# Performance work log

Hardware: AMD Instinct MI355X
Metric: run time of the kernel (lower is better)

The kernel has to match this reference:

```python
import jax, jax.numpy as jnp
import numpy as np

N = 50000      # nodes
E = 800000     # edges (before self-loops)
F_IN = 128
F_OUT = 128
H = 4          # heads
SLOPE = 0.2    # LeakyReLU negative slope (PyG GATConv default)


def setup_inputs() -> dict:
    key = jax.random.key(0)
    ks = jax.random.split(key, 8)
    x = jax.random.normal(ks[0], (N, F_IN), dtype=jnp.float32)
    edge_index = jax.random.randint(ks[1], (2, E), 0, N, dtype=jnp.int64)
    W = jax.random.normal(ks[2], (H, F_IN, F_OUT), dtype=jnp.float32) * (1.0 / np.sqrt(F_IN))
    att_src = jax.random.normal(ks[3], (H, F_OUT), dtype=jnp.float32) * (1.0 / np.sqrt(F_OUT))
    att_dst = jax.random.normal(ks[4], (H, F_OUT), dtype=jnp.float32) * (1.0 / np.sqrt(F_OUT))
    bias = jnp.zeros((H, F_OUT), dtype=jnp.float32)
    W_out = jax.random.normal(ks[5], (H * F_OUT, F_OUT), dtype=jnp.float32) * (1.0 / np.sqrt(H * F_OUT))
    b_out = jnp.zeros((F_OUT,), dtype=jnp.float32)
    return {"x": x, "edge_index": edge_index, "W": W, "att_src": att_src,
            "att_dst": att_dst, "bias": bias, "W_out": W_out, "b_out": b_out}


def _gat_head(x, src, dst, W_h, a_src, a_dst, b_h):
    # x: [N, F_in]; src/dst: [E'] edge endpoints (messages flow src -> dst)
    xW = x @ W_h                                   # [N, F_out]
    alpha_s = xW @ a_src                           # [N]
    alpha_d = xW @ a_dst                           # [N]
    logits = alpha_s[src] + alpha_d[dst]           # [E']
    logits = jnp.where(logits > 0, logits, SLOPE * logits)  # leaky_relu
    # segment softmax over edges grouped by destination node
    seg_max = jax.ops.segment_max(logits, dst, num_segments=N)  # [N]
    e = jnp.exp(logits - seg_max[dst])             # [E']
    denom = jax.ops.segment_sum(e, dst, num_segments=N)         # [N]
    alpha = e / denom[dst]                         # [E']
    # weighted scatter-aggregate of source features to destinations
    out = jax.ops.segment_sum(alpha[:, None] * xW[src], dst, num_segments=N)  # [N, F_out]
    return out + b_h


def reference(x, edge_index, W, att_src, att_dst, bias, W_out, b_out):
    # add self-loops (PyG GATConv default)
    loops = jnp.arange(N, dtype=edge_index.dtype)
    src = jnp.concatenate([edge_index[0], loops])
    dst = jnp.concatenate([edge_index[1], loops])
    heads = [_gat_head(x, src, dst, W[h], att_src[h], att_dst[h], bias[h]) for h in range(H)]
    h_cat = jnp.concatenate(heads, axis=1)         # [N, H*F_out]
    return jax.nn.relu(h_cat @ W_out + b_out)      # [N, F_out]
```

## Files before the change

### kernel.cpp

```cpp
#include <hip/hip_runtime.h>
#include <hip/hip_bf16.h>

constexpr int NN = 50000;
constexpr int EE = 800000;
constexpr float SLOPE = 0.2f;
constexpr int CAP = 48;
constexpr int ZE = NN * CAP;
constexpr int LDP = 520;

typedef __bf16 bf16x8 __attribute__((ext_vector_type(8)));
typedef __bf16 bf16x4 __attribute__((ext_vector_type(4)));
typedef float f32x4 __attribute__((ext_vector_type(4)));
typedef float f32x2 __attribute__((ext_vector_type(2)));

__device__ __forceinline__ int edge_at(const int* e32, const long long* e64, int use64, long i) {
    return use64 ? (int)e64[i] : e32[i];
}

__device__ __forceinline__ f32x2 bfpair(unsigned u) {
    f32x2 r;
    r.x = __uint_as_float(u << 16);
    r.y = __uint_as_float(u & 0xffff0000u);
    return r;
}

__global__ void k_prec(const float* __restrict__ W, const float* __restrict__ Wout,
                       const float* __restrict__ att_s, const float* __restrict__ att_d,
                       const float* __restrict__ bias, const float* __restrict__ bout,
                       const long long* e64, int* flag, int* cnt,
                       __bf16* __restrict__ Bfrag, float* __restrict__ wsv, float* __restrict__ wdv,
                       float* __restrict__ cvec, uint4* __restrict__ ew) {
    int b = blockIdx.x, t = threadIdx.x;
    if (b < 512) {
        int h = b >> 7, k = b & 127;
        float acc = 0.f;
        for (int j = 0; j < 128; j++) {
            float w = W[((size_t)(h * 128 + k)) * 128 + j];
            acc += w * Wout[((size_t)(h * 128 + j)) * 128 + t];
        }
        int K = h * 128 + k;
        int k0i = K >> 5, kb = (K >> 3) & 3, jj = K & 7;
        int ni = t >> 4, lr = t & 15;
        Bfrag[(((size_t)k0i * 8 + ni) * 64 + kb * 16 + lr) * 8 + jj] = (__bf16)acc;
    } else if (b == 512) {
        float acc = bout[t];
        for (int j = 0; j < 512; j++) acc += bias[j] * Wout[(size_t)j * 128 + t];
        cvec[t] = acc;
        if (t == 0) ew[ZE] = make_uint4(0u, 0u, 0u, 0u);
    } else if (b < 517) {
        int h = b - 513;
        float as = 0.f, ad = 0.f;
        for (int j = 0; j < 128; j++) {
            float w = W[((size_t)(h * 128 + t)) * 128 + j];
            as += w * att_s[h * 128 + j];
            ad += w * att_d[h * 128 + j];
        }
        wsv[h * 128 + t] = as;
        wdv[h * 128 + t] = ad;
    } else {
        int i = (b - 517) * 128 + t;
        if (i < NN) cnt[i] = 0;
        if (b == 517 && t < 64) {
            long long v = e64[t];
            bool ok = (v >= 0) && (v < (long long)NN);
            unsigned long long m = __ballot(ok);
            if (t == 0) *flag = (m == 0xFFFFFFFFFFFFFFFFull) ? 1 : 0;
        }
    }
}

__global__ __launch_bounds__(256) void k_prep(const float* __restrict__ x, const float* __restrict__ wsv,
                                              const float* __restrict__ wdv, __bf16* __restrict__ xb,
                                              float* __restrict__ as_, float* __restrict__ ad_) {
    int n = blockIdx.x * blockDim.x + threadIdx.x;
    if (n >= NN) return;
    const float4* xr = (const float4*)(x + (size_t)n * 128);
    __bf16* xo = xb + (size_t)n * 128;
    float s[4] = {0, 0, 0, 0}, d[4] = {0, 0, 0, 0};
    for (int q = 0; q < 32; q += 2) {
        float4 v0 = xr[q], v1 = xr[q + 1];
        bf16x8 o;
        o[0] = (__bf16)v0.x; o[1] = (__bf16)v0.y; o[2] = (__bf16)v0.z; o[3] = (__bf16)v0.w;
        o[4] = (__bf16)v1.x; o[5] = (__bf16)v1.y; o[6] = (__bf16)v1.z; o[7] = (__bf16)v1.w;
        *(bf16x8*)(xo + q * 4) = o;
        #pragma unroll
        for (int h = 0; h < 4; h++) {
            float4 a0 = ((const float4*)(wsv + h * 128))[q];
            float4 a1 = ((const float4*)(wsv + h * 128))[q + 1];
            float4 b0 = ((const float4*)(wdv + h * 128))[q];
            float4 b1 = ((const float4*)(wdv + h * 128))[q + 1];
            s[h] += v0.x * a0.x + v0.y * a0.y + v0.z * a0.z + v0.w * a0.w
                  + v1.x * a1.x + v1.y * a1.y + v1.z * a1.z + v1.w * a1.w;
            d[h] += v0.x * b0.x + v0.y * b0.y + v0.z * b0.z + v0.w * b0.w
                  + v1.x * b1.x + v1.y * b1.y + v1.z * b1.z + v1.w * b1.w;
        }
    }
    #pragma unroll
    for (int h = 0; h < 4; h++) { as_[n * 4 + h] = s[h]; ad_[n * 4 + h] = d[h]; }
}

__global__ __launch_bounds__(256) void k_scatterB(const int* e32, const long long* e64, const int* flag,
                                                  const float* __restrict__ as_, const float* __restrict__ ad_,
                                                  int* cnt, uint4* __restrict__ ew) {
    long i = (long)blockIdx.x * blockDim.x + threadIdx.x;
    if (i >= (long)EE + NN) return;
    int use64 = *flag;
    int s, d;
    if (i < EE) { s = edge_at(e32, e64, use64, i); d = edge_at(e32, e64, use64, (long)EE + i); }
    else        { s = (int)(i - EE); d = s; }
    float4 av = *(const float4*)(as_ + (size_t)s * 4);
    float4 bv = *(const float4*)(ad_ + (size_t)d * 4);
    float l0 = av.x + bv.x; l0 = l0 > 0.f ? l0 : SLOPE * l0;
    float l1 = av.y + bv.y; l1 = l1 > 0.f ? l1 : SLOPE * l1;
    float l2 = av.z + bv.z; l2 = l2 > 0.f ? l2 : SLOPE * l2;
    float l3 = av.w + bv.w; l3 = l3 > 0.f ? l3 : SLOPE * l3;
    bf16x4 w;
    w[0] = (__bf16)__expf(l0);
    w[1] = (__bf16)__expf(l1);
    w[2] = (__bf16)__expf(l2);
    w[3] = (__bf16)__expf(l3);
    uint2 wp = *(uint2*)&w;
    int pos = d * CAP + atomicAdd(&cnt[d], 1);
    ew[pos] = make_uint4((unsigned)s, wp.x, wp.y, 0u);
}

__global__ __launch_bounds__(256) void k_aggF(const int* __restrict__ cnt, const uint4* __restrict__ ew,
                                              const __bf16* __restrict__ xb, const __bf16* __restrict__ Bfrag,
                                              const float* __restrict__ cvec, float* __restrict__ y) {
    __shared__ __bf16 aggL[16 * LDP];
    int t = threadIdx.x;
    int lane = t & 63;
    int half = lane >> 5;
    int sub = lane & 31;
    int hw = ((t >> 6) << 1) + half;
    size_t fo = 4 * (size_t)sub;

    #pragma unroll
    for (int r = 0; r < 2; r++) {
        int nl = r * 8 + hw;
        int n = blockIdx.x * 16 + nl;
        int deg = cnt[n];
        int beg = n * CAP;
        int last = beg + deg - 1;
        int dmax = max(deg, __shfl_xor(deg, 32));
        int nit = (dmax + 3) >> 2;
        f32x2 a01[4] = {}, a23[4] = {};
        f32x2 dn01 = {0.f, 0.f}, dn23 = {0.f, 0.f};
        int e = beg;
        int i0 = (e     <= last) ? e     : ZE;
        int i1 = (e + 1 <= last) ? e + 1 : ZE;
        int i2 = (e + 2 <= last) ? e + 2 : ZE;
        int i3 = (e + 3 <= last) ? e + 3 : ZE;
        uint4 r0 = ew[i0], r1 = ew[i1], r2 = ew[i2], r3 = ew[i3];
        for (int it = 0; it < nit; ++it) {
            e += 4;
            int p0 = (e     <= last) ? e     : ZE;
            int p1 = (e + 1 <= last) ? e + 1 : ZE;
            int p2 = (e + 2 <= last) ? e + 2 : ZE;
            int p3 = (e + 3 <= last) ? e + 3 : ZE;
            uint4 n0 = ew[p0], n1 = ew[p1], n2 = ew[p2], n3 = ew[p3];
            uint2 x0 = *(const uint2*)(xb + (size_t)r0.x * 128 + fo);
            uint2 x1 = *(const uint2*)(xb + (size_t)r1.x * 128 + fo);
            uint2 x2 = *(const uint2*)(xb + (size_t)r2.x * 128 + fo);
            uint2 x3 = *(const uint2*)(xb + (size_t)r3.x * 128 + fo);
#define ACCP(R, XR) { \
            f32x2 w01 = bfpair(R.y), w23 = bfpair(R.z); \
            f32x2 x01 = bfpair(XR.x), x23 = bfpair(XR.y); \
            f32x2 q0 = {w01.x, w01.x}, q1 = {w01.y, w01.y}; \
            f32x2 q2 = {w23.x, w23.x}, q3 = {w23.y, w23.y}; \
            a01[0] += q0 * x01; a23[0] += q0 * x23; \
            a01[1] += q1 * x01; a23[1] += q1 * x23; \
            a01[2] += q2 * x01; a23[2] += q2 * x23; \
            a01[3] += q3 * x01; a23[3] += q3 * x23; \
            dn01 += w01; dn23 += w23; }
            ACCP(r0, x0) ACCP(r1, x1) ACCP(r2, x2) ACCP(r3, x3)
#undef ACCP
            r0 = n0; r1 = n1; r2 = n2; r3 = n3;
        }
        float inv[4];
        inv[0] = 1.f / dn01.x; inv[1] = 1.f / dn01.y;
        inv[2] = 1.f / dn23.x; inv[3] = 1.f / dn23.y;
        __bf16* ar = aggL + nl * LDP + fo;
        #pragma unroll
        for (int h = 0; h < 4; h++) {
            bf16x4 o;
            o[0] = (__bf16)(a01[h].x * inv[h]); o[1] = (__bf16)(a01[h].y * inv[h]);
            o[2] = (__bf16)(a23[h].x * inv[h]); o[3] = (__bf16)(a23[h].y * inv[h]);
            *(bf16x4*)(ar + h * 128) = o;
        }
    }
    __syncthreads();

    int w = t >> 6;
    int lr = lane & 15, kb = lane >> 4;
    f32x4 acc[2] = {};
    for (int k0i = 0; k0i < 16; k0i++) {
        bf16x8 a = *(const bf16x8*)(aggL + lr * LDP + k0i * 32 + kb * 8);
        #pragma unroll
        for (int ni = 0; ni < 2; ni++) {
            int ni_g = w * 2 + ni;
            bf16x8 b = *(const bf16x8*)(Bfrag + (((size_t)k0i * 8 + ni_g) * 64 + lane) * 8);
            acc[ni] = __builtin_amdgcn_mfma_f32_16x16x32_bf16(a, b, acc[ni], 0, 0, 0);
        }
    }
    int row0 = blockIdx.x * 16 + kb * 4;
    #pragma unroll
    for (int ni = 0; ni < 2; ni++) {
        int c = (w * 2 + ni) * 16 + lr;
        float cv = cvec[c];
        #pragma unroll
        for (int r = 0; r < 4; r++) {
            y[(size_t)(row0 + r) * 128 + c] = fmaxf(acc[ni][r] + cv, 0.f);
        }
    }
}

extern "C" void kernel_launch(void* const* d_in, const int* in_sizes, int n_in,
                              void* d_out, int out_size, void* d_ws, size_t ws_size,
                              hipStream_t stream) {
    const float* x     = (const float*)d_in[0];
    const void*  ei    = d_in[1];
    const float* W     = (const float*)d_in[2];
    const float* att_s = (const float*)d_in[3];
    const float* att_d = (const float*)d_in[4];
    const float* bias  = (const float*)d_in[5];
    const float* Wout  = (const float*)d_in[6];
    const float* bout  = (const float*)d_in[7];
    float* y = (float*)d_out;

    const int* e32 = (const int*)ei;
    const long long* e64 = (const long long*)ei;

    char* ws = (char*)d_ws;
    size_t off = 0;
    auto alloc = [&](size_t bytes) -> void* {
        void* p = ws + off;
        off = (off + bytes + 255) & ~(size_t)255;
        return p;
    };
    __bf16* xb    = (__bf16*)alloc((size_t)NN * 128 * 2);
    uint4* ew     = (uint4*)alloc(((size_t)NN * CAP + 1) * 16);
    float* as_    = (float*)alloc((size_t)NN * 4 * 4);
    float* ad_    = (float*)alloc((size_t)NN * 4 * 4);
    __bf16* Bfrag = (__bf16*)alloc((size_t)512 * 128 * 2);
    float* wsv    = (float*)alloc(4 * 128 * 4);
    float* wdv    = (float*)alloc(4 * 128 * 4);
    float* cvec   = (float*)alloc(128 * 4);
    int* cnt      = (int*)alloc((size_t)NN * 4);
    int* flag     = (int*)alloc(4);

    int precBlocks = 517 + (NN + 127) / 128;
    k_prec<<<precBlocks, 128, 0, stream>>>(W, Wout, att_s, att_d, bias, bout,
                                           e64, flag, cnt, Bfrag, wsv, wdv, cvec, ew);
    k_prep<<<(NN + 255) / 256, 256, 0, stream>>>(x, wsv, wdv, xb, as_, ad_);
    k_scatterB<<<(EE + NN + 255) / 256, 256, 0, stream>>>(e32, e64, flag, as_, ad_, cnt, ew);
    k_aggF<<<NN / 16, 256, 0, stream>>>(cnt, ew, xb, Bfrag, cvec, y);
}
```

Before: 139.3 us.

## Split edge scatter into index-only scatter plus per-node weight computation kernel

The edge scatter kernel now writes only the 4-byte source index into a per-destination slot array (capacity raised to 64, power-of-two indexing). A new kernel, one wavefront per destination node, reads those indices, gathers bf16 source attention scores, computes the exp-LeakyReLU weights, and writes the 16-byte edge records contiguously. This aims to make the random-atomic scatter pass lighter and turn weight writes into coalesced stores. In exchange it adds a kernel launch and an extra pass over the slots, stores source scores in bf16 (less precise), and uses more workspace for the larger capacity.

```diff
diff --git a/kernel.cpp b/kernel.cpp
--- a/kernel.cpp
+++ b/kernel.cpp
@@ -4,7 +4,7 @@
 constexpr int NN = 50000;
 constexpr int EE = 800000;
 constexpr float SLOPE = 0.2f;
-constexpr int CAP = 48;
+constexpr int CAP = 64;
 constexpr int ZE = NN * CAP;
 constexpr int LDP = 520;
 
@@ -71,7 +71,7 @@
 
 __global__ __launch_bounds__(256) void k_prep(const float* __restrict__ x, const float* __restrict__ wsv,
                                               const float* __restrict__ wdv, __bf16* __restrict__ xb,
-                                              float* __restrict__ as_, float* __restrict__ ad_) {
+                                              bf16x4* __restrict__ as_b, float* __restrict__ ad_) {
     int n = blockIdx.x * blockDim.x + threadIdx.x;
     if (n >= NN) return;
     const float4* xr = (const float4*)(x + (size_t)n * 128);
@@ -95,33 +95,47 @@
                   + v1.x * b1.x + v1.y * b1.y + v1.z * b1.z + v1.w * b1.w;
         }
     }
+    bf16x4 ab;
+    ab[0] = (__bf16)s[0]; ab[1] = (__bf16)s[1]; ab[2] = (__bf16)s[2]; ab[3] = (__bf16)s[3];
+    as_b[n] = ab;
     #pragma unroll
-    for (int h = 0; h < 4; h++) { as_[n * 4 + h] = s[h]; ad_[n * 4 + h] = d[h]; }
+    for (int h = 0; h < 4; h++) ad_[n * 4 + h] = d[h];
 }
 
 __global__ __launch_bounds__(256) void k_scatterB(const int* e32, const long long* e64, const int* flag,
-                                                  const float* __restrict__ as_, const float* __restrict__ ad_,
-                                                  int* cnt, uint4* __restrict__ ew) {
+                                                  int* cnt, int* __restrict__ colv) {
     long i = (long)blockIdx.x * blockDim.x + threadIdx.x;
     if (i >= (long)EE + NN) return;
     int use64 = *flag;
     int s, d;
     if (i < EE) { s = edge_at(e32, e64, use64, i); d = edge_at(e32, e64, use64, (long)EE + i); }
     else        { s = (int)(i - EE); d = s; }
-    float4 av = *(const float4*)(as_ + (size_t)s * 4);
-    float4 bv = *(const float4*)(ad_ + (size_t)d * 4);
-    float l0 = av.x + bv.x; l0 = l0 > 0.f ? l0 : SLOPE * l0;
-    float l1 = av.y + bv.y; l1 = l1 > 0.f ? l1 : SLOPE * l1;
-    float l2 = av.z + bv.z; l2 = l2 > 0.f ? l2 : SLOPE * l2;
-    float l3 = av.w + bv.w; l3 = l3 > 0.f ? l3 : SLOPE * l3;
+    int pos = (d << 6) + atomicAdd(&cnt[d], 1);
+    colv[pos] = s;
+}
+
+__global__ __launch_bounds__(256) void k_wcomp(const int* __restrict__ cnt, const int* __restrict__ colv,
+                                               const bf16x4* __restrict__ as_b, const float* __restrict__ ad_,
+                                               uint4* __restrict__ ew) {
+    int lane = threadIdx.x & 63;
+    int n = blockIdx.x * 4 + (threadIdx.x >> 6);
+    int deg = cnt[n];
+    if (lane >= deg) return;
+    int slot = (n << 6) + lane;
+    int src = colv[slot];
+    bf16x4 ab = as_b[src];
+    float4 adv = *(const float4*)(ad_ + (size_t)n * 4);
+    float l0 = (float)ab[0] + adv.x; l0 = l0 > 0.f ? l0 : SLOPE * l0;
+    float l1 = (float)ab[1] + adv.y; l1 = l1 > 0.f ? l1 : SLOPE * l1;
+    float l2 = (float)ab[2] + adv.z; l2 = l2 > 0.f ? l2 : SLOPE * l2;
+    float l3 = (float)ab[3] + adv.w; l3 = l3 > 0.f ? l3 : SLOPE * l3;
     bf16x4 w;
     w[0] = (__bf16)__expf(l0);
     w[1] = (__bf16)__expf(l1);
     w[2] = (__bf16)__expf(l2);
     w[3] = (__bf16)__expf(l3);
     uint2 wp = *(uint2*)&w;
-    int pos = d * CAP + atomicAdd(&cnt[d], 1);
-    ew[pos] = make_uint4((unsigned)s, wp.x, wp.y, 0u);
+    ew[slot] = make_uint4((unsigned)src, wp.x, wp.y, 0u);
 }
 
 __global__ __launch_bounds__(256) void k_aggF(const int* __restrict__ cnt, const uint4* __restrict__ ew,
@@ -140,7 +154,7 @@
         int nl = r * 8 + hw;
         int n = blockIdx.x * 16 + nl;
         int deg = cnt[n];
-        int beg = n * CAP;
+        int beg = n << 6;
         int last = beg + deg - 1;
         int dmax = max(deg, __shfl_xor(deg, 32));
         int nit = (dmax + 3) >> 2;
@@ -240,7 +254,8 @@
     };
     __bf16* xb    = (__bf16*)alloc((size_t)NN * 128 * 2);
     uint4* ew     = (uint4*)alloc(((size_t)NN * CAP + 1) * 16);
-    float* as_    = (float*)alloc((size_t)NN * 4 * 4);
+    int* colv     = (int*)alloc((size_t)NN * CAP * 4);
+    bf16x4* as_b  = (bf16x4*)alloc((size_t)NN * 8);
     float* ad_    = (float*)alloc((size_t)NN * 4 * 4);
     __bf16* Bfrag = (__bf16*)alloc((size_t)512 * 128 * 2);
     float* wsv    = (float*)alloc(4 * 128 * 4);
@@ -252,7 +267,8 @@
     int precBlocks = 517 + (NN + 127) / 128;
     k_prec<<<precBlocks, 128, 0, stream>>>(W, Wout, att_s, att_d, bias, bout,
                                            e64, flag, cnt, Bfrag, wsv, wdv, cvec, ew);
-    k_prep<<<(NN + 255) / 256, 256, 0, stream>>>(x, wsv, wdv, xb, as_, ad_);
-    k_scatterB<<<(EE + NN + 255) / 256, 256, 0, stream>>>(e32, e64, flag, as_, ad_, cnt, ew);
+    k_prep<<<(NN + 255) / 256, 256, 0, stream>>>(x, wsv, wdv, xb, as_b, ad_);
+    k_scatterB<<<(EE + NN + 255) / 256, 256, 0, stream>>>(e32, e64, flag, cnt, colv);
+    k_wcomp<<<NN / 4, 256, 0, stream>>>(cnt, colv, as_b, ad_, ew);
     k_aggF<<<NN / 16, 256, 0, stream>>>(cnt, ew, xb, Bfrag, cvec, y);
 }
```

Result: slower. 156.3 us (+12.2%).

## Fuse weight precompute and node prep into one front kernel, widen bucket capacity

Applied to the files above, without the earlier changes.

The separate attention-vector precompute and the node prep kernel are merged into one launch. Each prep block recomputes W·att_src and W·att_dst into shared memory, which removes a kernel launch and its dependency barrier at the cost of redundant per-block GEMV work. The per-node edge bucket capacity goes from 48 to 64 so slot indexing can use shifts, at the cost of a larger edge buffer. The aggregation loop also drops its software prefetch of edge records, which lowers register pressure but exposes load latency.

```diff
diff --git a/kernel.cpp b/kernel.cpp
--- a/kernel.cpp
+++ b/kernel.cpp
@@ -4,9 +4,10 @@
 constexpr int NN = 50000;
 constexpr int EE = 800000;
 constexpr float SLOPE = 0.2f;
-constexpr int CAP = 48;
+constexpr int CAP = 64;
 constexpr int ZE = NN * CAP;
 constexpr int LDP = 520;
+constexpr int NB = (NN + 127) / 128;
 
 typedef __bf16 bf16x8 __attribute__((ext_vector_type(8)));
 typedef __bf16 bf16x4 __attribute__((ext_vector_type(4)));
@@ -24,12 +25,14 @@
     return r;
 }
 
-__global__ void k_prec(const float* __restrict__ W, const float* __restrict__ Wout,
-                       const float* __restrict__ att_s, const float* __restrict__ att_d,
-                       const float* __restrict__ bias, const float* __restrict__ bout,
-                       const long long* e64, int* flag, int* cnt,
-                       __bf16* __restrict__ Bfrag, float* __restrict__ wsv, float* __restrict__ wdv,
-                       float* __restrict__ cvec, uint4* __restrict__ ew) {
+__global__ __launch_bounds__(128) void k_front(const float* __restrict__ W, const float* __restrict__ Wout,
+                                               const float* __restrict__ att_s, const float* __restrict__ att_d,
+                                               const float* __restrict__ bias, const float* __restrict__ bout,
+                                               const float* __restrict__ x, const long long* e64,
+                                               int* flag, int* cnt,
+                                               __bf16* __restrict__ Bfrag, float* __restrict__ cvec,
+                                               uint4* __restrict__ ew, __bf16* __restrict__ xb,
+                                               float* __restrict__ as_, float* __restrict__ ad_) {
     int b = blockIdx.x, t = threadIdx.x;
     if (b < 512) {
         int h = b >> 7, k = b & 127;
@@ -47,56 +50,58 @@
         for (int j = 0; j < 512; j++) acc += bias[j] * Wout[(size_t)j * 128 + t];
         cvec[t] = acc;
         if (t == 0) ew[ZE] = make_uint4(0u, 0u, 0u, 0u);
-    } else if (b < 517) {
-        int h = b - 513;
-        float as = 0.f, ad = 0.f;
-        for (int j = 0; j < 128; j++) {
-            float w = W[((size_t)(h * 128 + t)) * 128 + j];
-            as += w * att_s[h * 128 + j];
-            ad += w * att_d[h * 128 + j];
-        }
-        wsv[h * 128 + t] = as;
-        wdv[h * 128 + t] = ad;
-    } else {
-        int i = (b - 517) * 128 + t;
+    } else if (b < 513 + NB) {
+        int i = (b - 513) * 128 + t;
         if (i < NN) cnt[i] = 0;
-        if (b == 517 && t < 64) {
+        if (b == 513 && t < 64) {
             long long v = e64[t];
             bool ok = (v >= 0) && (v < (long long)NN);
             unsigned long long m = __ballot(ok);
             if (t == 0) *flag = (m == 0xFFFFFFFFFFFFFFFFull) ? 1 : 0;
         }
-    }
-}
-
-__global__ __launch_bounds__(256) void k_prep(const float* __restrict__ x, const float* __restrict__ wsv,
-                                              const float* __restrict__ wdv, __bf16* __restrict__ xb,
-                                              float* __restrict__ as_, float* __restrict__ ad_) {
-    int n = blockIdx.x * blockDim.x + threadIdx.x;
-    if (n >= NN) return;
-    const float4* xr = (const float4*)(x + (size_t)n * 128);
-    __bf16* xo = xb + (size_t)n * 128;
-    float s[4] = {0, 0, 0, 0}, d[4] = {0, 0, 0, 0};
-    for (int q = 0; q < 32; q += 2) {
-        float4 v0 = xr[q], v1 = xr[q + 1];
-        bf16x8 o;
-        o[0] = (__bf16)v0.x; o[1] = (__bf16)v0.y; o[2] = (__bf16)v0.z; o[3] = (__bf16)v0.w;
-        o[4] = (__bf16)v1.x; o[5] = (__bf16)v1.y; o[6] = (__bf16)v1.z; o[7] = (__bf16)v1.w;
-        *(bf16x8*)(xo + q * 4) = o;
+    } else {
+        __shared__ float wsvL[4 * 128], wdvL[4 * 128];
         #pragma unroll
         for (int h = 0; h < 4; h++) {
-            float4 a0 = ((const float4*)(wsv + h * 128))[q];
-            float4 a1 = ((const float4*)(wsv + h * 128))[q + 1];
-            float4 b0 = ((const float4*)(wdv + h * 128))[q];
-            float4 b1 = ((const float4*)(wdv + h * 128))[q + 1];
-            s[h] += v0.x * a0.x + v0.y * a0.y + v0.z * a0.z + v0.w * a0.w
-                  + v1.x * a1.x + v1.y * a1.y + v1.z * a1.z + v1.w * a1.w;
-            d[h] += v0.x * b0.x + v0.y * b0.y + v0.z * b0.z + v0.w * b0.w
-                  + v1.x * b1.x + v1.y * b1.y + v1.z * b1.z + v1.w * b1.w;
-        }
-    }
-    #pragma unroll
-    for (int h = 0; h < 4; h++) { as_[n * 4 + h] = s[h]; ad_[n * 4 + h] = d[h]; }
+            float as = 0.f, ad = 0.f;
+            const float4* wr = (const float4*)(W + ((size_t)(h * 128 + t)) * 128);
+            const float4* ar = (const float4*)(att_s + h * 128);
+            const float4* br = (const float4*)(att_d + h * 128);
+            for (int j = 0; j < 32; j++) {
+                float4 w4 = wr[j], a4 = ar[j], b4 = br[j];
+                as += w4.x * a4.x + w4.y * a4.y + w4.z * a4.z + w4.w * a4.w;
+                ad += w4.x * b4.x + w4.y * b4.y + w4.z * b4.z + w4.w * b4.w;
+            }
+            wsvL[h * 128 + t] = as;
+            wdvL[h * 128 + t] = ad;
+        }
+        __syncthreads();
+        int n = (b - 513 - NB) * 128 + t;
+        if (n >= NN) return;
+        const float4* xr = (const float4*)(x + (size_t)n * 128);
+        __bf16* xo = xb + (size_t)n * 128;
+        float s[4] = {0, 0, 0, 0}, d[4] = {0, 0, 0, 0};
+        for (int q = 0; q < 32; q += 2) {
+            float4 v0 = xr[q], v1 = xr[q + 1];
+            bf16x8 o;
+            o[0] = (__bf16)v0.x; o[1] = (__bf16)v0.y; o[2] = (__bf16)v0.z; o[3] = (__bf16)v0.w;
+            o[4] = (__bf16)v1.x; o[5] = (__bf16)v1.y; o[6] = (__bf16)v1.z; o[7] = (__bf16)v1.w;
+            *(bf16x8*)(xo + q * 4) = o;
+            #pragma unroll
+            for (int h = 0; h < 4; h++) {
+                float4 a0 = ((const float4*)(wsvL + h * 128))[q];
+                float4 a1 = ((const float4*)(wsvL + h * 128))[q + 1];
+                float4 b0 = ((const float4*)(wdvL + h * 128))[q];
+                float4 b1 = ((const float4*)(wdvL + h * 128))[q + 1];
+                s[h] += v0.x * a0.x + v0.y * a0.y + v0.z * a0.z + v0.w * a0.w
+                      + v1.x * a1.x + v1.y * a1.y + v1.z * a1.z + v1.w * a1.w;
+                d[h] += v0.x * b0.x + v0.y * b0.y + v0.z * b0.z + v0.w * b0.w
+                      + v1.x * b1.x + v1.y * b1.y + v1.z * b1.z + v1.w * b1.w;
+            }
+        }
+        #pragma unroll
+        for (int h = 0; h < 4; h++) { as_[n * 4 + h] = s[h]; ad_[n * 4 + h] = d[h]; }
+    }
 }
 
 __global__ __launch_bounds__(256) void k_scatterB(const int* e32, const long long* e64, const int* flag,
@@ -120,7 +125,7 @@
     w[2] = (__bf16)__expf(l2);
     w[3] = (__bf16)__expf(l3);
     uint2 wp = *(uint2*)&w;
-    int pos = d * CAP + atomicAdd(&cnt[d], 1);
+    int pos = (d << 6) + atomicAdd(&cnt[d], 1);
     ew[pos] = make_uint4((unsigned)s, wp.x, wp.y, 0u);
 }
 
@@ -140,25 +145,19 @@
         int nl = r * 8 + hw;
         int n = blockIdx.x * 16 + nl;
         int deg = cnt[n];
-        int beg = n * CAP;
+        int beg = n << 6;
         int last = beg + deg - 1;
         int dmax = max(deg, __shfl_xor(deg, 32));
         int nit = (dmax + 3) >> 2;
         f32x2 a01[4] = {}, a23[4] = {};
         f32x2 dn01 = {0.f, 0.f}, dn23 = {0.f, 0.f};
         int e = beg;
-        int i0 = (e     <= last) ? e     : ZE;
-        int i1 = (e + 1 <= last) ? e + 1 : ZE;
-        int i2 = (e + 2 <= last) ? e + 2 : ZE;
-        int i3 = (e + 3 <= last) ? e + 3 : ZE;
-        uint4 r0 = ew[i0], r1 = ew[i1], r2 = ew[i2], r3 = ew[i3];
-        for (int it = 0; it < nit; ++it) {
-            e += 4;
-            int p0 = (e     <= last) ? e     : ZE;
-            int p1 = (e + 1 <= last) ? e + 1 : ZE;
-            int p2 = (e + 2 <= last) ? e + 2 : ZE;
-            int p3 = (e + 3 <= last) ? e + 3 : ZE;
-            uint4 n0 = ew[p0], n1 = ew[p1], n2 = ew[p2], n3 = ew[p3];
+        for (int it = 0; it < nit; ++it, e += 4) {
+            int i0 = (e     <= last) ? e     : ZE;
+            int i1 = (e + 1 <= last) ? e + 1 : ZE;
+            int i2 = (e + 2 <= last) ? e + 2 : ZE;
+            int i3 = (e + 3 <= last) ? e + 3 : ZE;
+            uint4 r0 = ew[i0], r1 = ew[i1], r2 = ew[i2], r3 = ew[i3];
             uint2 x0 = *(const uint2*)(xb + (size_t)r0.x * 128 + fo);
             uint2 x1 = *(const uint2*)(xb + (size_t)r1.x * 128 + fo);
             uint2 x2 = *(const uint2*)(xb + (size_t)r2.x * 128 + fo);
@@ -175,7 +174,6 @@
             dn01 += w01; dn23 += w23; }
             ACCP(r0, x0) ACCP(r1, x1) ACCP(r2, x2) ACCP(r3, x3)
 #undef ACCP
-            r0 = n0; r1 = n1; r2 = n2; r3 = n3;
         }
         float inv[4];
         inv[0] = 1.f / dn01.x; inv[1] = 1.f / dn01.y;
@@ -243,16 +241,13 @@
     float* as_    = (float*)alloc((size_t)NN * 4 * 4);
     float* ad_    = (float*)alloc((size_t)NN * 4 * 4);
     __bf16* Bfrag = (__bf16*)alloc((size_t)512 * 128 * 2);
-    float* wsv    = (float*)alloc(4 * 128 * 4);
-    float* wdv    = (float*)alloc(4 * 128 * 4);
     float* cvec   = (float*)alloc(128 * 4);
     int* cnt      = (int*)alloc((size_t)NN * 4);
     int* flag     = (int*)alloc(4);
 
-    int precBlocks = 517 + (NN + 127) / 128;
-    k_prec<<<precBlocks, 128, 0, stream>>>(W, Wout, att_s, att_d, bias, bout,
-                                           e64, flag, cnt, Bfrag, wsv, wdv, cvec, ew);
-    k_prep<<<(NN + 255) / 256, 256, 0, stream>>>(x, wsv, wdv, xb, as_, ad_);
+    int frontBlocks = 513 + NB + NB;
+    k_front<<<frontBlocks, 128, 0, stream>>>(W, Wout, att_s, att_d, bias, bout, x, e64,
+                                             flag, cnt, Bfrag, cvec, ew, xb, as_, ad_);
     k_scatterB<<<(EE + NN + 255) / 256, 256, 0, stream>>>(e32, e64, flag, as_, ad_, cnt, ew);
     k_aggF<<<NN / 16, 256, 0, stream>>>(cnt, ew, xb, Bfrag, cvec, y);
 }
```

New measurement: 129.7 us (median of 2 runs). -7.0%, faster.
